# Optimization experiments

Measured on AMD Instinct MI355X. Metric: run time of the kernel, lower is better.

## Reference

```python
import jax, jax.numpy as jnp
import numpy as np

N, D, B = 500000, 128, 2048

def setup_inputs() -> dict:
    key = jax.random.key(0)
    ks = jax.random.split(key, 7)
    x = jax.random.normal(ks[0], (N, D), dtype=jnp.float32)
    batch = jnp.sort(jax.random.randint(ks[1], (N,), 0, B)).astype(jnp.int64)
    s = 1.0 / np.sqrt(D)
    Wm = jax.random.uniform(ks[2], (D, D), jnp.float32, -s, s)  # xavier-ish
    fc1_w = jax.random.uniform(ks[3], (D // 4, D), jnp.float32, -s, s)
    fc1_b = jnp.zeros((D // 4,), jnp.float32)
    fc2_w = jax.random.uniform(ks[4], (D, D // 4), jnp.float32, -1/np.sqrt(D//4), 1/np.sqrt(D//4))
    fc2_b = jnp.zeros((D,), jnp.float32)
    return {"x": x, "batch": batch, "size": B, "Wm": Wm,
            "fc1_w": fc1_w, "fc1_b": fc1_b, "fc2_w": fc2_w, "fc2_b": fc2_b}

def reference(x, batch, size, Wm, fc1_w, fc1_b, fc2_w, fc2_b):
    batch = batch.astype(jnp.int32)
    # fc: Linear -> ReLU -> Linear -> Tanh
    attention = jnp.tanh(jax.nn.relu(x @ fc1_w.T + fc1_b) @ fc2_w.T + fc2_b)
    x2 = attention * x + x  # [N, D]
    # scatter_mean over graphs
    sums = jax.ops.segment_sum(x2, batch, num_segments=size)  # [B, D]
    cnt = jax.ops.segment_sum(jnp.ones((x2.shape[0],), x2.dtype), batch, num_segments=size)
    mean = sums / jnp.maximum(cnt, 1.0)[:, None]
    transformed_global = jnp.tanh(mean @ Wm)  # [B, D]
    coefs = jax.nn.sigmoid(jnp.sum(x2 * transformed_global[batch], axis=1))  # [N]
    weighted = coefs[:, None] * x2
    return jax.ops.segment_sum(weighted, batch, num_segments=size)  # [B, D]
```

## Files before the change

kernel.cpp:

```cpp
#include <hip/hip_runtime.h>
#include <math.h>

#define D 128
#define BLOCKS_A 768
#define BLOCKS_C 1024
#define THREADS 256

typedef short s8v __attribute__((ext_vector_type(8)));
typedef float f4v __attribute__((ext_vector_type(4)));

__device__ __forceinline__ float fast_tanh(float z) {
    float e = __expf(2.f * z);
    return 1.f - 2.f / (e + 1.f);
}
__device__ __forceinline__ unsigned cvt_pk_bf16(float lo, float hi) {
    unsigned r;
    asm("v_cvt_pk_bf16_f32 %0, %1, %2" : "=v"(r) : "v"(lo), "v"(hi));
    return r;
}
__device__ __forceinline__ float bf2f(unsigned short h) {
    union { unsigned u; float f; } v; v.u = ((unsigned)h) << 16;
    return v.f;
}
__device__ __forceinline__ s8v pack8(float4 w0, float4 w1) {
    union { unsigned u[4]; s8v v; } r;
    r.u[0] = cvt_pk_bf16(w0.x, w0.y);
    r.u[1] = cvt_pk_bf16(w0.z, w0.w);
    r.u[2] = cvt_pk_bf16(w1.x, w1.y);
    r.u[3] = cvt_pk_bf16(w1.z, w1.w);
    return r.v;
}

#define EPI0(RG_)                                                             \
    {                                                                         \
        int r = R + quad * 4 + RG_;                                           \
        int seg = batch[r];                                                   \
        float yv[8];                                                          \
        _Pragma("unroll")                                                     \
        for (int t = 0; t < 8; ++t) {                                         \
            float xf = bf2f(xw[(quad * 4 + RG_) * 136 + m15 + 16 * t]);       \
            float z = af[t][RG_] + b2l[t];                                    \
            yv[t] = xf * (1.f + fast_tanh(z));                                \
        }                                                                     \
        union { unsigned u[4]; uint4 q; } pk;                                 \
        pk.u[0] = cvt_pk_bf16(yv[0], yv[1]);                                  \
        pk.u[1] = cvt_pk_bf16(yv[2], yv[3]);                                  \
        pk.u[2] = cvt_pk_bf16(yv[4], yv[5]);                                  \
        pk.u[3] = cvt_pk_bf16(yv[6], yv[7]);                                  \
        ((uint4*)x2s)[(size_t)b * 256 + RG_ * 64 + lane] = pk.q;              \
        if (seg != cur) {                                                     \
            if (cur >= 0) {                                                   \
                _Pragma("unroll")                                             \
                for (int t = 0; t < 8; ++t)                                   \
                    atomicAdd(&sums[cur * 128 + m15 + 16 * t], acc[t]);       \
                if (m15 == 0) atomicAdd(&cnt[cur], acnt);                     \
            }                                                                 \
            cur = seg;                                                        \
            _Pragma("unroll")                                                 \
            for (int t = 0; t < 8; ++t) acc[t] = yv[t];                       \
            acnt = 1.f;                                                       \
        } else {                                                              \
            _Pragma("unroll")                                                 \
            for (int t = 0; t < 8; ++t) acc[t] += yv[t];                      \
            acnt += 1.f;                                                      \
        }                                                                     \
    }

__global__ __launch_bounds__(THREADS, 2) void phaseA(
    const float* __restrict__ x, const int* __restrict__ batch,
    const float* __restrict__ fc1_w, const float* __restrict__ fc1_b,
    const float* __restrict__ fc2_w, const float* __restrict__ fc2_b,
    float* __restrict__ sums, float* __restrict__ cnt,
    unsigned short* __restrict__ x2s, int N)
{
    __shared__ unsigned short xbf[4][16 * 136];
    __shared__ float hbuf[4][16 * 36];

    const int lane = threadIdx.x & 63;
    const int wv = threadIdx.x >> 6;
    const int m15 = lane & 15;
    const int quad = lane >> 4;

    s8v B1[2][4];
    #pragma unroll
    for (int t = 0; t < 2; ++t)
        #pragma unroll
        for (int kc = 0; kc < 4; ++kc) {
            const float* p = fc1_w + (16 * t + m15) * 128 + kc * 32 + quad * 8;
            B1[t][kc] = pack8(*(const float4*)p, *(const float4*)(p + 4));
        }
    s8v B2[8];
    #pragma unroll
    for (int t = 0; t < 8; ++t) {
        const float* p = fc2_w + (16 * t + m15) * 32 + quad * 8;
        B2[t] = pack8(*(const float4*)p, *(const float4*)(p + 4));
    }
    float b1l[2], b2l[8];
    #pragma unroll
    for (int t = 0; t < 2; ++t) b1l[t] = fc1_b[m15 + 16 * t];
    #pragma unroll
    for (int t = 0; t < 8; ++t) b2l[t] = fc2_b[m15 + 16 * t];

    const int total16 = N >> 4;
    const int nw = BLOCKS_A * 4;
    const int gw = blockIdx.x * 4 + wv;
    const int base = total16 / nw, rem = total16 % nw;
    const int b0 = gw * base + (gw < rem ? gw : rem);
    const int b1e = b0 + base + (gw < rem ? 1 : 0);

    unsigned short* xw = xbf[wv];
    float* hw = hbuf[wv];

    float acc[8];
    #pragma unroll
    for (int t = 0; t < 8; ++t) acc[t] = 0.f;
    int cur = -1;
    float acnt = 0.f;
    const f4v z4 = {0.f, 0.f, 0.f, 0.f};

    float4 L[8];
    if (b0 < b1e) {
        const float* xp = x + (size_t)(b0 << 4) * D;
        #pragma unroll
        for (int u = 0; u < 8; ++u)
            L[u] = *(const float4*)(xp + u * 256 + lane * 4);
    }

    for (int b = b0; b < b1e; ++b) {
        const int R = b << 4;
        uint2 P[8];
        #pragma unroll
        for (int u = 0; u < 8; ++u) {
            P[u].x = cvt_pk_bf16(L[u].x, L[u].y);
            P[u].y = cvt_pk_bf16(L[u].z, L[u].w);
        }
        if (b + 1 < b1e) {
            const float* xp = x + (size_t)((b + 1) << 4) * D;
            #pragma unroll
            for (int u = 0; u < 8; ++u)
                L[u] = *(const float4*)(xp + u * 256 + lane * 4);
        }
        #pragma unroll
        for (int u = 0; u < 8; ++u) {
            int row = 2 * u + (lane >> 5);
            int col = (lane & 31) * 4;
            *(uint2*)&xw[row * 136 + col] = P[u];
        }
        s8v ax[4];
        #pragma unroll
        for (int kc = 0; kc < 4; ++kc)
            ax[kc] = *(const s8v*)&xw[m15 * 136 + kc * 32 + quad * 8];
        f4v accH[2];
        accH[0] = z4; accH[1] = z4;
        #pragma unroll
        for (int kc = 0; kc < 4; ++kc) {
            accH[0] = __builtin_amdgcn_mfma_f32_16x16x32_bf16(ax[kc], B1[0][kc], accH[0], 0, 0, 0);
            accH[1] = __builtin_amdgcn_mfma_f32_16x16x32_bf16(ax[kc], B1[1][kc], accH[1], 0, 0, 0);
        }
        #pragma unroll
        for (int t = 0; t < 2; ++t)
            #pragma unroll
            for (int rg = 0; rg < 4; ++rg) {
                float hv = fmaxf(accH[t][rg] + b1l[t], 0.f);
                hw[(quad * 4 + rg) * 36 + m15 + 16 * t] = hv;
            }
        const f4v h0 = *(const f4v*)&hw[m15 * 36 + quad * 8];
        const f4v h1 = *(const f4v*)&hw[m15 * 36 + quad * 8 + 4];
        union { unsigned u[4]; s8v v; } ahu;
        ahu.u[0] = cvt_pk_bf16(h0[0], h0[1]);
        ahu.u[1] = cvt_pk_bf16(h0[2], h0[3]);
        ahu.u[2] = cvt_pk_bf16(h1[0], h1[1]);
        ahu.u[3] = cvt_pk_bf16(h1[2], h1[3]);
        s8v ah = ahu.v;
        f4v af[8];
        #pragma unroll
        for (int t = 0; t < 8; ++t)
            af[t] = __builtin_amdgcn_mfma_f32_16x16x32_bf16(ah, B2[t], z4, 0, 0, 0);

        EPI0(0) EPI0(1) EPI0(2) EPI0(3)
    }
    if (cur >= 0) {
        #pragma unroll
        for (int t = 0; t < 8; ++t)
            atomicAdd(&sums[cur * 128 + m15 + 16 * t], acc[t]);
        if (m15 == 0) atomicAdd(&cnt[cur], acnt);
    }
}

__global__ __launch_bounds__(D, 8) void phaseB(
    const float* __restrict__ sums, const float* __restrict__ cnt,
    const float* __restrict__ Wm, float* __restrict__ tg)
{
    int b = blockIdx.x;
    int d = threadIdx.x;
    __shared__ float m[D];
    float inv = 1.f / fmaxf(cnt[b], 1.f);
    m[d] = sums[(b << 7) + d] * inv;
    __syncthreads();
    float acc = 0.f;
    #pragma unroll 8
    for (int k = 0; k < D; ++k)
        acc = fmaf(m[k], Wm[(k << 7) + d], acc);
    tg[(b << 7) + d] = fast_tanh(acc);
}

__global__ __launch_bounds__(THREADS, 4) void phaseC(
    const unsigned short* __restrict__ x2s, const int* __restrict__ batch,
    const float* __restrict__ tg, float* __restrict__ out, int N)
{
    const int lane = threadIdx.x & 63;
    const int wv = threadIdx.x >> 6;
    const int m15 = lane & 15;
    const int quad = lane >> 4;

    const int total16 = N >> 4;
    const int nw = BLOCKS_C * 4;
    const int gw = blockIdx.x * 4 + wv;
    const int base = total16 / nw, rem = total16 % nw;
    const int b0 = gw * base + (gw < rem ? gw : rem);
    const int b1e = b0 + base + (gw < rem ? 1 : 0);

    float acc[8], tgv[8];
    #pragma unroll
    for (int t = 0; t < 8; ++t) { acc[t] = 0.f; tgv[t] = 0.f; }
    int cur = -1;

    uint4 PK[4];
    if (b0 < b1e) {
        const uint4* p = (const uint4*)x2s + (size_t)b0 * 256 + lane;
        #pragma unroll
        for (int rg = 0; rg < 4; ++rg) PK[rg] = p[rg * 64];
    }

    for (int b = b0; b < b1e; ++b) {
        uint4 C[4];
        #pragma unroll
        for (int rg = 0; rg < 4; ++rg) C[rg] = PK[rg];
        if (b + 1 < b1e) {
            const uint4* p = (const uint4*)x2s + (size_t)(b + 1) * 256 + lane;
            #pragma unroll
            for (int rg = 0; rg < 4; ++rg) PK[rg] = p[rg * 64];
        }
        const int R = b << 4;
        #pragma unroll
        for (int rg = 0; rg < 4; ++rg) {
            int seg = batch[R + quad * 4 + rg];
            if (seg != cur) {
                if (cur >= 0) {
                    #pragma unroll
                    for (int t = 0; t < 8; ++t)
                        atomicAdd(&out[cur * 128 + m15 + 16 * t], acc[t]);
                }
                cur = seg;
                #pragma unroll
                for (int t = 0; t < 8; ++t) {
                    tgv[t] = tg[seg * 128 + m15 + 16 * t];
                    acc[t] = 0.f;
                }
            }
            float xv[8];
            unsigned w;
            union { unsigned u; float f; } cv;
            w = C[rg].x; cv.u = w << 16; xv[0] = cv.f; cv.u = w & 0xffff0000u; xv[1] = cv.f;
            w = C[rg].y; cv.u = w << 16; xv[2] = cv.f; cv.u = w & 0xffff0000u; xv[3] = cv.f;
            w = C[rg].z; cv.u = w << 16; xv[4] = cv.f; cv.u = w & 0xffff0000u; xv[5] = cv.f;
            w = C[rg].w; cv.u = w << 16; xv[6] = cv.f; cv.u = w & 0xffff0000u; xv[7] = cv.f;
            float dot = 0.f;
            #pragma unroll
            for (int t = 0; t < 8; ++t) dot = fmaf(xv[t], tgv[t], dot);
            dot += __shfl_xor(dot, 1);
            dot += __shfl_xor(dot, 2);
            dot += __shfl_xor(dot, 4);
            dot += __shfl_xor(dot, 8);
            float coef = 1.f / (1.f + __expf(-dot));
            #pragma unroll
            for (int t = 0; t < 8; ++t) acc[t] = fmaf(coef, xv[t], acc[t]);
        }
    }
    if (cur >= 0) {
        #pragma unroll
        for (int t = 0; t < 8; ++t)
            atomicAdd(&out[cur * 128 + m15 + 16 * t], acc[t]);
    }
}

extern "C" void kernel_launch(void* const* d_in, const int* in_sizes, int n_in,
                              void* d_out, int out_size, void* d_ws, size_t ws_size,
                              hipStream_t stream) {
    const float* x     = (const float*)d_in[0];
    const int*   batch = (const int*)d_in[1];
    const float* Wm    = (const float*)d_in[3];
    const float* fc1_w = (const float*)d_in[4];
    const float* fc1_b = (const float*)d_in[5];
    const float* fc2_w = (const float*)d_in[6];
    const float* fc2_b = (const float*)d_in[7];
    float* out = (float*)d_out;

    int N = in_sizes[0] / D;
    int B = out_size / D;

    float* sums = (float*)d_ws;
    float* cnt  = sums + (size_t)B * D;
    float* tg   = cnt + B;
    unsigned short* x2s = (unsigned short*)(tg + (size_t)B * D);

    hipMemsetAsync(d_ws, 0, ((size_t)B * D + B) * sizeof(float), stream);
    hipMemsetAsync(d_out, 0, (size_t)out_size * sizeof(float), stream);

    phaseA<<<BLOCKS_A, THREADS, 0, stream>>>(
        x, batch, fc1_w, fc1_b, fc2_w, fc2_b, sums, cnt, x2s, N);
    phaseB<<<B, D, 0, stream>>>(sums, cnt, Wm, tg);
    phaseC<<<BLOCKS_C, THREADS, 0, stream>>>(x2s, batch, tg, out, N);
}
```

Before: 465.5 us.

## Load x directly in MFMA layout, move weights to LDS, raise occupancy

```diff
diff --git a/kernel.cpp b/kernel.cpp
--- a/kernel.cpp
+++ b/kernel.cpp
@@ -3,7 +3,7 @@
 
 #define D 128
 #define BLOCKS_A 768
-#define BLOCKS_C 1024
+#define BLOCKS_C 1536
 #define THREADS 256
 
 typedef short s8v __attribute__((ext_vector_type(8)));
@@ -17,10 +17,6 @@
     unsigned r;
     asm("v_cvt_pk_bf16_f32 %0, %1, %2" : "=v"(r) : "v"(lo), "v"(hi));
     return r;
-}
-__device__ __forceinline__ float bf2f(unsigned short h) {
-    union { unsigned u; float f; } v; v.u = ((unsigned)h) << 16;
-    return v.f;
 }
 __device__ __forceinline__ s8v pack8(float4 w0, float4 w1) {
     union { unsigned u[4]; s8v v; } r;
@@ -35,12 +31,12 @@
     {                                                                         \
         int r = R + quad * 4 + RG_;                                           \
         int seg = batch[r];                                                   \
+        const float* xrow = x + (size_t)r * 128 + m15;                        \
         float yv[8];                                                          \
         _Pragma("unroll")                                                     \
         for (int t = 0; t < 8; ++t) {                                         \
-            float xf = bf2f(xw[(quad * 4 + RG_) * 136 + m15 + 16 * t]);       \
             float z = af[t][RG_] + b2l[t];                                    \
-            yv[t] = xf * (1.f + fast_tanh(z));                                \
+            yv[t] = xrow[16 * t] * (1.f + fast_tanh(z));                      \
         }                                                                     \
         union { unsigned u[4]; uint4 q; } pk;                                 \
         pk.u[0] = cvt_pk_bf16(yv[0], yv[1]);                                  \
@@ -66,14 +62,15 @@
         }                                                                     \
     }
 
-__global__ __launch_bounds__(THREADS, 2) void phaseA(
+__global__ __launch_bounds__(THREADS, 3) void phaseA(
     const float* __restrict__ x, const int* __restrict__ batch,
     const float* __restrict__ fc1_w, const float* __restrict__ fc1_b,
     const float* __restrict__ fc2_w, const float* __restrict__ fc2_b,
     float* __restrict__ sums, float* __restrict__ cnt,
     unsigned short* __restrict__ x2s, int N)
 {
-    __shared__ unsigned short xbf[4][16 * 136];
+    __shared__ s8v wB1[2][4][64];
+    __shared__ s8v wB2[8][64];
     __shared__ float hbuf[4][16 * 36];
 
     const int lane = threadIdx.x & 63;
@@ -81,25 +78,26 @@
     const int m15 = lane & 15;
     const int quad = lane >> 4;
 
-    s8v B1[2][4];
-    #pragma unroll
-    for (int t = 0; t < 2; ++t)
-        #pragma unroll
-        for (int kc = 0; kc < 4; ++kc) {
-            const float* p = fc1_w + (16 * t + m15) * 128 + kc * 32 + quad * 8;
-            B1[t][kc] = pack8(*(const float4*)p, *(const float4*)(p + 4));
-        }
-    s8v B2[8];
-    #pragma unroll
-    for (int t = 0; t < 8; ++t) {
-        const float* p = fc2_w + (16 * t + m15) * 32 + quad * 8;
-        B2[t] = pack8(*(const float4*)p, *(const float4*)(p + 4));
+    if (wv == 0) {
+        #pragma unroll
+        for (int t = 0; t < 2; ++t)
+            #pragma unroll
+            for (int kc = 0; kc < 4; ++kc) {
+                const float* p = fc1_w + (16 * t + m15) * 128 + kc * 32 + quad * 8;
+                wB1[t][kc][lane] = pack8(*(const float4*)p, *(const float4*)(p + 4));
+            }
+        #pragma unroll
+        for (int t = 0; t < 8; ++t) {
+            const float* p = fc2_w + (16 * t + m15) * 32 + quad * 8;
+            wB2[t][lane] = pack8(*(const float4*)p, *(const float4*)(p + 4));
+        }
     }
     float b1l[2], b2l[8];
     #pragma unroll
     for (int t = 0; t < 2; ++t) b1l[t] = fc1_b[m15 + 16 * t];
     #pragma unroll
     for (int t = 0; t < 8; ++t) b2l[t] = fc2_b[m15 + 16 * t];
+    __syncthreads();
 
     const int total16 = N >> 4;
     const int nw = BLOCKS_A * 4;
@@ -108,7 +106,6 @@
     const int b0 = gw * base + (gw < rem ? gw : rem);
     const int b1e = b0 + base + (gw < rem ? 1 : 0);
 
-    unsigned short* xw = xbf[wv];
     float* hw = hbuf[wv];
 
     float acc[8];
@@ -118,44 +115,36 @@
     float acnt = 0.f;
     const f4v z4 = {0.f, 0.f, 0.f, 0.f};
 
-    float4 L[8];
+    float4 F[8];
     if (b0 < b1e) {
-        const float* xp = x + (size_t)(b0 << 4) * D;
-        #pragma unroll
-        for (int u = 0; u < 8; ++u)
-            L[u] = *(const float4*)(xp + u * 256 + lane * 4);
+        const float* xp = x + (size_t)(b0 << 4) * D + m15 * 128 + quad * 8;
+        #pragma unroll
+        for (int kc = 0; kc < 4; ++kc) {
+            F[2 * kc]     = *(const float4*)(xp + kc * 32);
+            F[2 * kc + 1] = *(const float4*)(xp + kc * 32 + 4);
+        }
     }
 
     for (int b = b0; b < b1e; ++b) {
         const int R = b << 4;
-        uint2 P[8];
-        #pragma unroll
-        for (int u = 0; u < 8; ++u) {
-            P[u].x = cvt_pk_bf16(L[u].x, L[u].y);
-            P[u].y = cvt_pk_bf16(L[u].z, L[u].w);
-        }
+        s8v ax[4];
+        #pragma unroll
+        for (int kc = 0; kc < 4; ++kc)
+            ax[kc] = pack8(F[2 * kc], F[2 * kc + 1]);
         if (b + 1 < b1e) {
-            const float* xp = x + (size_t)((b + 1) << 4) * D;
-            #pragma unroll
-            for (int u = 0; u < 8; ++u)
-                L[u] = *(const float4*)(xp + u * 256 + lane * 4);
-        }
-        #pragma unroll
-        for (int u = 0; u < 8; ++u) {
-            int row = 2 * u + (lane >> 5);
-            int col = (lane & 31) * 4;
-            *(uint2*)&xw[row * 136 + col] = P[u];
-        }
-        s8v ax[4];
-        #pragma unroll
-        for (int kc = 0; kc < 4; ++kc)
-            ax[kc] = *(const s8v*)&xw[m15 * 136 + kc * 32 + quad * 8];
+            const float* xp = x + (size_t)((b + 1) << 4) * D + m15 * 128 + quad * 8;
+            #pragma unroll
+            for (int kc = 0; kc < 4; ++kc) {
+                F[2 * kc]     = *(const float4*)(xp + kc * 32);
+                F[2 * kc + 1] = *(const float4*)(xp + kc * 32 + 4);
+            }
+        }
         f4v accH[2];
         accH[0] = z4; accH[1] = z4;
         #pragma unroll
         for (int kc = 0; kc < 4; ++kc) {
-            accH[0] = __builtin_amdgcn_mfma_f32_16x16x32_bf16(ax[kc], B1[0][kc], accH[0], 0, 0, 0);
-            accH[1] = __builtin_amdgcn_mfma_f32_16x16x32_bf16(ax[kc], B1[1][kc], accH[1], 0, 0, 0);
+            accH[0] = __builtin_amdgcn_mfma_f32_16x16x32_bf16(ax[kc], wB1[0][kc][lane], accH[0], 0, 0, 0);
+            accH[1] = __builtin_amdgcn_mfma_f32_16x16x32_bf16(ax[kc], wB1[1][kc][lane], accH[1], 0, 0, 0);
         }
         #pragma unroll
         for (int t = 0; t < 2; ++t)
@@ -175,7 +164,7 @@
         f4v af[8];
         #pragma unroll
         for (int t = 0; t < 8; ++t)
-            af[t] = __builtin_amdgcn_mfma_f32_16x16x32_bf16(ah, B2[t], z4, 0, 0, 0);
+            af[t] = __builtin_amdgcn_mfma_f32_16x16x32_bf16(ah, wB2[t][lane], z4, 0, 0, 0);
 
         EPI0(0) EPI0(1) EPI0(2) EPI0(3)
     }
@@ -204,7 +193,7 @@
     tg[(b << 7) + d] = fast_tanh(acc);
 }
 
-__global__ __launch_bounds__(THREADS, 4) void phaseC(
+__global__ __launch_bounds__(THREADS, 6) void phaseC(
     const unsigned short* __restrict__ x2s, const int* __restrict__ batch,
     const float* __restrict__ tg, float* __restrict__ out, int N)
 {
@@ -225,26 +214,18 @@
     for (int t = 0; t < 8; ++t) { acc[t] = 0.f; tgv[t] = 0.f; }
     int cur = -1;
 
-    uint4 PK[4];
-    if (b0 < b1e) {
-        const uint4* p = (const uint4*)x2s + (size_t)b0 * 256 + lane;
-        #pragma unroll
-        for (int rg = 0; rg < 4; ++rg) PK[rg] = p[rg * 64];
-    }
-
     for (int b = b0; b < b1e; ++b) {
-        uint4 C[4];
-        #pragma unroll
-        for (int rg = 0; rg < 4; ++rg) C[rg] = PK[rg];
-        if (b + 1 < b1e) {
-            const uint4* p = (const uint4*)x2s + (size_t)(b + 1) * 256 + lane;
-            #pragma unroll
-            for (int rg = 0; rg < 4; ++rg) PK[rg] = p[rg * 64];
-        }
         const int R = b << 4;
+        const uint4* p = (const uint4*)x2s + (size_t)b * 256 + lane;
+        uint4 C0 = p[0], C1 = p[64], C2 = p[128], C3 = p[192];
+        int sg0 = batch[R + quad * 4 + 0];
+        int sg1 = batch[R + quad * 4 + 1];
+        int sg2 = batch[R + quad * 4 + 2];
+        int sg3 = batch[R + quad * 4 + 3];
         #pragma unroll
         for (int rg = 0; rg < 4; ++rg) {
-            int seg = batch[R + quad * 4 + rg];
+            uint4 C = rg == 0 ? C0 : rg == 1 ? C1 : rg == 2 ? C2 : C3;
+            int seg = rg == 0 ? sg0 : rg == 1 ? sg1 : rg == 2 ? sg2 : sg3;
             if (seg != cur) {
                 if (cur >= 0) {
                     #pragma unroll
@@ -261,10 +242,10 @@
             float xv[8];
             unsigned w;
             union { unsigned u; float f; } cv;
-            w = C[rg].x; cv.u = w << 16; xv[0] = cv.f; cv.u = w & 0xffff0000u; xv[1] = cv.f;
-            w = C[rg].y; cv.u = w << 16; xv[2] = cv.f; cv.u = w & 0xffff0000u; xv[3] = cv.f;
-            w = C[rg].z; cv.u = w << 16; xv[4] = cv.f; cv.u = w & 0xffff0000u; xv[5] = cv.f;
-            w = C[rg].w; cv.u = w << 16; xv[6] = cv.f; cv.u = w & 0xffff0000u; xv[7] = cv.f;
+            w = C.x; cv.u = w << 16; xv[0] = cv.f; cv.u = w & 0xffff0000u; xv[1] = cv.f;
+            w = C.y; cv.u = w << 16; xv[2] = cv.f; cv.u = w & 0xffff0000u; xv[3] = cv.f;
+            w = C.z; cv.u = w << 16; xv[4] = cv.f; cv.u = w & 0xffff0000u; xv[5] = cv.f;
+            w = C.w; cv.u = w << 16; xv[6] = cv.f; cv.u = w & 0xffff0000u; xv[7] = cv.f;
             float dot = 0.f;
             #pragma unroll
             for (int t = 0; t < 8; ++t) dot = fmaf(xv[t], tgv[t], dot);
```

Result: slower. 475.1 us (+2.1%).
